# Kernel tuning notes

Measured on AMD Instinct MI355X. Metric: run time of the kernel, lower is better.

The kernel has to match this reference:

```python
import jax, jax.numpy as jnp
import numpy as np

B, T, V, S, I, G = 2, 4096, 1024, 256, 2048, 128


def setup_inputs() -> dict:
    key = jax.random.key(0)
    ks = jax.random.split(key, 10)
    n = lambda k, shape, std: jax.random.normal(k, shape, dtype=jnp.float32) * std
    return {
        "x": jax.random.normal(ks[0], (B, T, V), dtype=jnp.float32),
        # shared CausalMemory projections (torch Linear weight layout [out,in])
        "Wq": n(ks[1], (S, V), 0.02),
        "Wk": n(ks[2], (S, V), 0.02),
        "Wv": n(ks[3], (S, V), 0.02),
        "Wo": n(ks[4], (V, S), 0.02),
        # Delta
        "delta_logits": jnp.full((V,), 4.0, dtype=jnp.float32),
        "delta_scale": jnp.float32(0.1),
        # Theta / Gamma decay params
        "theta_decay": jnp.float32(4.0),
        "theta_scale": jnp.float32(0.1),
        "gamma_decay": jnp.float32(1.0),
        "gamma_scale": jnp.float32(0.1),
        # Alpha gate
        "alpha_down": n(ks[5], (G, V), 0.02),
        "alpha_up": n(ks[6], (V, G), 0.01),
        "alpha_up_b": jnp.full((V,), 2.0, dtype=jnp.float32),
        # Beta MLP
        "beta_down": n(ks[7], (I, V), 0.02),
        "beta_up": n(ks[8], (V, I), 0.02),
        "beta_bias": jnp.zeros((I,), dtype=jnp.float32),
        "beta_scale": jnp.float32(0.1),
    }


def _rmsnorm(x):
    eps = jnp.finfo(x.dtype).eps
    return x * jax.lax.rsqrt(jnp.mean(x * x, axis=-1, keepdims=True) + eps)


def _delta(x, decay_logits, scale):
    # causal EMA via weighted cumsum, matching torch reference exactly
    t = x.shape[1]
    decay = jax.nn.sigmoid(decay_logits)
    log_decay = jnp.log(jnp.clip(decay, 1e-06))
    steps = jnp.arange(t, dtype=x.dtype)[::-1]            # [T]
    w = jnp.exp(steps[:, None] * log_decay[None, :])      # [T,V]
    cum = jnp.cumsum(x * w[None], axis=1)
    cum = jnp.concatenate([jnp.zeros_like(cum[:, :1]), cum[:, :-1]], axis=1)
    return cum / jnp.clip(w[None], 1e-08) * scale


def _memory(x, Wq, Wk, Wv, Wo, decay_logit, scale):
    t = x.shape[1]
    q = x @ Wq.T
    k = x @ Wk.T
    v = x @ Wv.T
    scores = jnp.einsum("btd,bsd->bts", q, k)             # [B,T,T]
    decay = jax.nn.sigmoid(decay_logit)
    pos = jnp.arange(t)
    diff = pos[None, :] - pos[:, None]                    # j - i
    w = decay ** jnp.clip(diff.astype(x.dtype) - 1.0, 0.0, None) * (diff > 0)
    retrieved = jnp.einsum("bts,bsd->btd", scores * w[None], v)
    return (retrieved @ Wo.T) * scale


def _alpha(x, down, up, up_b):
    gate = jax.nn.sigmoid((x @ down.T) @ up.T + up_b)
    return x * gate


def _beta(x, down, up, bias, scale):
    h = jax.nn.gelu(x @ down.T + bias, approximate=False)
    return (h @ up.T) * scale


def reference(x, Wq, Wk, Wv, Wo, delta_logits, delta_scale, theta_decay,
              theta_scale, gamma_decay, gamma_scale, alpha_down, alpha_up,
              alpha_up_b, beta_down, beta_up, beta_bias, beta_scale):
    x = x + _delta(_rmsnorm(x), delta_logits, delta_scale)
    x = x + _memory(_rmsnorm(x), Wq, Wk, Wv, Wo, theta_decay, theta_scale)
    x = _alpha(x, alpha_down, alpha_up, alpha_up_b)
    x = x + _beta(_rmsnorm(x), beta_down, beta_up, beta_bias, beta_scale)
    x = x + _memory(_rmsnorm(x), Wq, Wk, Wv, Wo, gamma_decay, gamma_scale)
    return x
```

## Files before the change

### kernel.cpp

```cpp
#include <hip/hip_runtime.h>

typedef __attribute__((ext_vector_type(8))) short s16x8;
typedef __attribute__((ext_vector_type(4))) float f32x4;
typedef unsigned short u16;

#define DEV __device__ __forceinline__

DEV u16 f2b(float f) {
  unsigned u = __builtin_bit_cast(unsigned, f);
  unsigned r = (u + 0x7FFFu + ((u >> 16) & 1u)) >> 16;
  return (u16)r;
}
DEV float b2f(u16 h) { return __builtin_bit_cast(float, (unsigned)h << 16); }
DEV f32x4 mfma16(s16x8 a, s16x8 b, f32x4 c) {
  return __builtin_amdgcn_mfma_f32_16x16x32_bf16(a, b, c, 0, 0, 0);
}
DEV float sigmoidf_(float x) { return 1.0f / (1.0f + expf(-x)); }

DEV void g2l16(const u16* g, u16* l) {
  __builtin_amdgcn_global_load_lds((const __attribute__((address_space(1))) void*)g,
                                   (__attribute__((address_space(3))) void*)l, 16, 0, 0);
}

#define BAR() __builtin_amdgcn_s_barrier()
#define WAITV8() asm volatile("s_waitcnt vmcnt(8)" ::: "memory")
#define WAITV4() asm volatile("s_waitcnt vmcnt(4)" ::: "memory")
#define WAITV0() asm volatile("s_waitcnt vmcnt(0)" ::: "memory")
#define WAITL0()                                         \
  do {                                                   \
    asm volatile("s_waitcnt lgkmcnt(0)" ::: "memory");   \
    __builtin_amdgcn_sched_barrier(0);                   \
  } while (0)

__global__ __launch_bounds__(256) void cast_all(
    const float* __restrict__ Wq, const float* __restrict__ Wk, const float* __restrict__ Wv,
    const float* __restrict__ Wo, const float* __restrict__ adw, const float* __restrict__ auw,
    const float* __restrict__ bdw, const float* __restrict__ buw,
    u16* __restrict__ Wqkvb, u16* __restrict__ Wob, u16* __restrict__ adb,
    u16* __restrict__ aub, u16* __restrict__ bdb, u16* __restrict__ bub) {
  const int b = blockIdx.x;
  const float* s;
  u16* d;
  int rb;
  if (b < 768) {
    s = (b < 256) ? Wq : (b < 512) ? Wk : Wv;
    rb = (b < 256) ? b : (b < 512) ? (b - 256) : (b - 512);
    d = Wqkvb + ((b < 256) ? 0 : (b < 512) ? 262144 : 524288);
  } else if (b < 1024) { s = Wo;  d = Wob; rb = b - 768; }
  else if (b < 1152)   { s = adw; d = adb; rb = b - 1024; }
  else if (b < 1280)   { s = auw; d = aub; rb = b - 1152; }
  else if (b < 3328)   { s = bdw; d = bdb; rb = b - 1280; }
  else                 { s = buw; d = bub; rb = b - 3328; }
  size_t i = ((size_t)rb * 256 + threadIdx.x) * 4;
  float4 v = *(const float4*)(s + i);
  ushort4 p; p.x = f2b(v.x); p.y = f2b(v.y); p.z = f2b(v.z); p.w = f2b(v.w);
  *(ushort4*)(d + i) = p;
}

__global__ __launch_bounds__(256) void rmsnorm_k(const float* __restrict__ x, u16* __restrict__ y) {
  const size_t row = blockIdx.x;
  const int tid = threadIdx.x;
  float4 v = ((const float4*)(x + row * 1024))[tid];
  float ss = v.x * v.x + v.y * v.y + v.z * v.z + v.w * v.w;
#pragma unroll
  for (int o = 32; o >= 1; o >>= 1) ss += __shfl_xor(ss, o);
  __shared__ float red[4];
  if ((tid & 63) == 0) red[tid >> 6] = ss;
  __syncthreads();
  float tot = red[0] + red[1] + red[2] + red[3];
  float rn = rsqrtf(tot * (1.0f / 1024.0f) + 1.1920929e-7f);
  ushort4 p;
  p.x = f2b(v.x * rn); p.y = f2b(v.y * rn); p.z = f2b(v.z * rn); p.w = f2b(v.w * rn);
  *(ushort4*)(y + row * 1024 + tid * 4) = p;
}

__global__ __launch_bounds__(256)
void delta_partial(const u16* __restrict__ y, const float* __restrict__ logits, float* __restrict__ Pp) {
  const int v = blockIdx.x * 256 + threadIdx.x;
  const int c = blockIdx.y, b = blockIdx.z;
  const float dec = sigmoidf_(logits[v]);
  const float ldc = logf(fmaxf(dec, 1e-6f));
  const float dc = expf(ldc);
  const u16* yp = y + ((size_t)b * 4096 + c * 128) * 1024 + v;
  float wv = expf((float)(4095 - (c * 128 + 127)) * ldc);
  float acc = 0.0f;
  for (int t = 127; t >= 0; --t) {
    acc += b2f(yp[(size_t)t * 1024]) * wv;
    wv *= dc;
  }
  Pp[((size_t)b * 32 + c) * 1024 + v] = acc;
}

__global__ __launch_bounds__(256) void delta_scan(float* __restrict__ Pp) {
  const int v = blockIdx.x * 256 + threadIdx.x;
  const int b = blockIdx.y;
  float run = 0.0f;
  for (int c = 0; c < 32; ++c) {
    size_t i = ((size_t)b * 32 + c) * 1024 + v;
    float t = Pp[i];
    Pp[i] = run;
    run += t;
  }
}

__global__ __launch_bounds__(256)
void delta_apply(const float* __restrict__ x0, const u16* __restrict__ y,
                 const float* __restrict__ logits, const float* __restrict__ scale_p,
                 const float* __restrict__ Pp, float* __restrict__ x1) {
  const int v = blockIdx.x * 256 + threadIdx.x;
  const int c = blockIdx.y, b = blockIdx.z;
  const float dec = sigmoidf_(logits[v]);
  const float ldc = logf(fmaxf(dec, 1e-6f));
  const float dc = expf(ldc);
  const float invd = expf(-ldc);
  const float sc = scale_p[0];
  float wv = expf((float)(4095 - c * 128) * ldc);
  float iw = expf(-(float)(4095 - c * 128) * ldc);
  float carry = Pp[((size_t)b * 32 + c) * 1024 + v];
  size_t base = ((size_t)b * 4096 + c * 128) * 1024 + v;
  for (int t = 0; t < 128; ++t) {
    size_t idx = base + (size_t)t * 1024;
    x1[idx] = x0[idx] + carry * fminf(iw, 1e8f) * sc;
    carry += b2f(y[idx]) * wv;
    wv *= invd;
    iw *= dc;
  }
}

template <int EPI>
__global__ __launch_bounds__(256, 4)
void pgemm_s(const u16* __restrict__ A, const u16* __restrict__ Bw,
             int M, int N, int K,
             u16* __restrict__ Cb,
             const float* __restrict__ Xin, float* __restrict__ Xout,
             u16* __restrict__ Xb16,
             const float* __restrict__ bias, const float* __restrict__ scale_p,
             u16* __restrict__ P1, u16* __restrict__ P2, u16* __restrict__ P3) {
  __shared__ u16 sm[17472];
  const int tid = threadIdx.x;
  const int wid = tid >> 6, lane = tid & 63;
  const int gx = gridDim.x;
  const int id = blockIdx.y * gx + blockIdx.x;
  const int q8 = (gx * gridDim.y) >> 3;
  const int nid = (id & 7) * q8 + (id >> 3);
  const int bx = nid % gx, by = nid / gx;
  const int n0 = bx * 128, m0 = by * 128;
  const int wm = (wid >> 1) * 64, wn = (wid & 1) * 64;
  const int lr = lane & 15, lkc = lane >> 4;
  const int sw = lr & 7;
  const int c0 = (lkc ^ sw) * 8, c1 = ((lkc + 4) ^ sw) * 8;
  const int NT = K >> 6;
  const int srow = lane >> 3;
  const int scol = ((lane & 7) ^ srow) * 8;
  const u16* Ag = A + (size_t)(m0 + wid * 8 + srow) * K + scol;
  const u16* Bg = Bw + (size_t)(n0 + wid * 8 + srow) * K + scol;
  u16* const As = sm;
  u16* const Bs = sm + 8192;

  f32x4 acc[4][4] = {};

  for (int t = 0; t < NT; ++t) {
    {
      const u16* ga = Ag + (size_t)t * 64;
      const u16* gb = Bg + (size_t)t * 64;
      u16* la = As + wid * 512;
      u16* lb = Bs + wid * 512;
#pragma unroll
      for (int c = 0; c < 4; ++c) {
        g2l16(ga + (size_t)c * 32 * K, la + c * 2048);
        g2l16(gb + (size_t)c * 32 * K, lb + c * 2048);
      }
    }
    __syncthreads();
    s16x8 af[4][2], bfr[2][2][2];
#pragma unroll
    for (int i = 0; i < 4; ++i) {
      int base = (wm + i * 16 + lr) * 64;
      af[i][0] = *(const s16x8*)&As[base + c0];
      af[i][1] = *(const s16x8*)&As[base + c1];
    }
#pragma unroll
    for (int h = 0; h < 2; ++h)
#pragma unroll
      for (int j = 0; j < 2; ++j) {
        int base = (wn + h * 32 + j * 16 + lr) * 64;
        bfr[h][j][0] = *(const s16x8*)&Bs[base + c0];
        bfr[h][j][1] = *(const s16x8*)&Bs[base + c1];
      }
#pragma unroll
    for (int i = 0; i < 4; ++i)
#pragma unroll
      for (int h = 0; h < 2; ++h)
#pragma unroll
        for (int j = 0; j < 2; ++j) {
          acc[i][h * 2 + j] = mfma16(af[i][0], bfr[h][j][0], acc[i][h * 2 + j]);
          acc[i][h * 2 + j] = mfma16(af[i][1], bfr[h][j][1], acc[i][h * 2 + j]);
        }
    __syncthreads();
  }

  float* tl = (float*)(void*)sm + wid * 1088;

  if constexpr (EPI == 5) {
    if (bx < 4) {
      u16* dst = (bx < 2) ? Cb : P1;
      const int nb = (bx & 1) * 128;
#pragma unroll
      for (int i = 0; i < 4; ++i) {
#pragma unroll
        for (int j = 0; j < 4; ++j)
#pragma unroll
          for (int r = 0; r < 4; ++r)
            tl[(lkc * 4 + r) * 68 + j * 16 + lr] = acc[i][j][r];
#pragma unroll
        for (int p = 0; p < 4; ++p) {
          const int row = p * 4 + lkc, nl = lr * 4;
          f32x4 v = *(const f32x4*)&tl[row * 68 + nl];
          const int m = m0 + wm + i * 16 + row;
          ushort4 o = {f2b(v[0]), f2b(v[1]), f2b(v[2]), f2b(v[3])};
          *(ushort4*)&dst[(size_t)m * 256 + nb + wn + nl] = o;
        }
      }
      if (bx >= 2) {
        const float ld5 = logf(sigmoidf_(scale_p[0]));
        u16* CT = sm;
        __syncthreads();
#pragma unroll
        for (int i = 0; i < 4; ++i)
#pragma unroll
          for (int j = 0; j < 4; ++j)
#pragma unroll
            for (int r = 0; r < 4; ++r) {
              int ml = wm + i * 16 + lkc * 4 + r;
              int nl = wn + j * 16 + lr;
              float g = expf(ld5 * (float)(ml & 63));
              CT[nl * 136 + ml] = f2b(acc[i][j][r] * g);
            }
        __syncthreads();
        int d = tid >> 1, off = (tid & 1) * 64;
        size_t base = ((size_t)(m0 >> 12) * 256 + (bx - 2) * 128 + d) * 4096 + (m0 & 4095) + off;
#pragma unroll
        for (int p = 0; p < 8; ++p)
          *(uint4*)&P3[base + p * 8] = *(const uint4*)&CT[d * 136 + off + p * 8];
      }
    } else {
      u16* CT = sm;
      __syncthreads();
#pragma unroll
      for (int i = 0; i < 4; ++i)
#pragma unroll
        for (int j = 0; j < 4; ++j)
#pragma unroll
          for (int r = 0; r < 4; ++r) {
            int ml = wm + i * 16 + lkc * 4 + r;
            int nl = wn + j * 16 + lr;
            CT[nl * 136 + ml] = f2b(acc[i][j][r]);
          }
      __syncthreads();
      int d = tid >> 1, off = (tid & 1) * 64;
      size_t base = ((size_t)(m0 >> 12) * 256 + (bx - 4) * 128 + d) * 4096 + (m0 & 4095) + off;
#pragma unroll
      for (int p = 0; p < 8; ++p)
        *(uint4*)&P2[base + p * 8] = *(const uint4*)&CT[d * 136 + off + p * 8];
    }
  } else {
    const float sc = (EPI == 2) ? scale_p[0] : 0.0f;
    float4 bpf = {0.0f, 0.0f, 0.0f, 0.0f};
    if constexpr (EPI == 3 || EPI == 4) bpf = *(const float4*)&bias[n0 + wn + lr * 4];
#pragma unroll
    for (int i = 0; i < 4; ++i) {
#pragma unroll
      for (int j = 0; j < 4; ++j)
#pragma unroll
        for (int r = 0; r < 4; ++r)
          tl[(lkc * 4 + r) * 68 + j * 16 + lr] = acc[i][j][r];
#pragma unroll
      for (int p = 0; p < 4; ++p) {
        const int row = p * 4 + lkc, nl = lr * 4;
        f32x4 v = *(const f32x4*)&tl[row * 68 + nl];
        const int m = m0 + wm + i * 16 + row;
        const int n = n0 + wn + nl;
        const size_t idx = (size_t)m * N + n;
        if constexpr (EPI == 0) {
          ushort4 o = {f2b(v[0]), f2b(v[1]), f2b(v[2]), f2b(v[3])};
          *(ushort4*)&Cb[idx] = o;
        } else if constexpr (EPI == 2) {
          float4 x = *(const float4*)&Xin[idx];
          float4 o = {x.x + v[0] * sc, x.y + v[1] * sc, x.z + v[2] * sc, x.w + v[3] * sc};
          *(float4*)&Xout[idx] = o;
          if (Xb16) {
            ushort4 ob = {f2b(o.x), f2b(o.y), f2b(o.z), f2b(o.w)};
            *(ushort4*)&Xb16[idx] = ob;
          }
        } else if constexpr (EPI == 3) {
          float g0 = v[0] + bpf.x, g1 = v[1] + bpf.y, g2 = v[2] + bpf.z, g3 = v[3] + bpf.w;
          ushort4 o;
          o.x = f2b(g0 * sigmoidf_(1.59576912f * fmaf(0.044715f * g0, g0 * g0, g0)));
          o.y = f2b(g1 * sigmoidf_(1.59576912f * fmaf(0.044715f * g1, g1 * g1, g1)));
          o.z = f2b(g2 * sigmoidf_(1.59576912f * fmaf(0.044715f * g2, g2 * g2, g2)));
          o.w = f2b(g3 * sigmoidf_(1.59576912f * fmaf(0.044715f * g3, g3 * g3, g3)));
          *(ushort4*)&Cb[idx] = o;
        } else {
          float4 x = *(const float4*)&Xin[idx];
          float4 o = {x.x * sigmoidf_(v[0] + bpf.x), x.y * sigmoidf_(v[1] + bpf.y),
                      x.z * sigmoidf_(v[2] + bpf.z), x.w * sigmoidf_(v[3] + bpf.w)};
          *(float4*)&Xout[idx] = o;
        }
      }
    }
  }
}

template <int EPI>
__global__ __launch_bounds__(256, 2)
void pgemm_d(const u16* __restrict__ A, const u16* __restrict__ Bw,
             int M, int N, int K,
             u16* __restrict__ Cb,
             const float* __restrict__ Xin, float* __restrict__ Xout,
             u16* __restrict__ Xb16,
             const float* __restrict__ bias, const float* __restrict__ scale_p) {
  __shared__ u16 sm[32768];
  const int tid = threadIdx.x;
  const int wid = tid >> 6, lane = tid & 63;
  const int gx = gridDim.x;
  const int id = blockIdx.y * gx + blockIdx.x;
  const int q8 = (gx * gridDim.y) >> 3;
  const int nid = (id & 7) * q8 + (id >> 3);
  const int bx = nid % gx, by = nid / gx;
  const int n0 = bx * 128, m0 = by * 128;
  const int wm = (wid >> 1) * 64, wn = (wid & 1) * 64;
  const int lr = lane & 15, lkc = lane >> 4;
  const int sw = lr & 7;
  const int c0 = (lkc ^ sw) * 8, c1 = ((lkc + 4) ^ sw) * 8;
  const int NT = K >> 6;
  const int srow = lane >> 3;
  const int scol = ((lane & 7) ^ srow) * 8;
  const u16* Ag = A + (size_t)(m0 + wid * 8 + srow) * K + scol;
  const u16* Bg = Bw + (size_t)(n0 + wid * 8 + srow) * K + scol;
  u16* const AL0 = sm;          u16* const BL0 = sm + 8192;
  u16* const AL1 = sm + 16384;  u16* const BL1 = sm + 24576;

  f32x4 acc[4][4] = {};

  auto STA = [&](int tau) {
    const u16* g = Ag + (size_t)tau * 64;
    u16* l = ((tau & 1) ? AL1 : AL0) + wid * 512;
#pragma unroll
    for (int c = 0; c < 4; ++c) g2l16(g + (size_t)c * 32 * K, l + c * 2048);
  };
  auto STB = [&](int tau) {
    const u16* g = Bg + (size_t)tau * 64;
    u16* l = ((tau & 1) ? BL1 : BL0) + wid * 512;
#pragma unroll
    for (int c = 0; c < 4; ++c) g2l16(g + (size_t)c * 32 * K, l + c * 2048);
  };
  auto RDA = [&](int tau, s16x8 (&d)[4][2]) {
    const u16* Ab = (tau & 1) ? AL1 : AL0;
#pragma unroll
    for (int i = 0; i < 4; ++i) {
      int base = (wm + i * 16 + lr) * 64;
      d[i][0] = *(const s16x8*)&Ab[base + c0];
      d[i][1] = *(const s16x8*)&Ab[base + c1];
    }
  };
  auto RDB = [&](int tau, int h, s16x8 (&d)[2][2]) {
    const u16* Bb = (tau & 1) ? BL1 : BL0;
#pragma unroll
    for (int j = 0; j < 2; ++j) {
      int base = (wn + h * 32 + j * 16 + lr) * 64;
      d[j][0] = *(const s16x8*)&Bb[base + c0];
      d[j][1] = *(const s16x8*)&Bb[base + c1];
    }
  };
  auto MM = [&](s16x8 (&Ar)[4][2], s16x8 (&Br)[2][2], int jo) {
    __builtin_amdgcn_s_setprio(1);
#pragma unroll
    for (int i = 0; i < 4; ++i)
#pragma unroll
      for (int j = 0; j < 2; ++j) {
        acc[i][jo + j] = mfma16(Ar[i][0], Br[j][0], acc[i][jo + j]);
        acc[i][jo + j] = mfma16(Ar[i][1], Br[j][1], acc[i][jo + j]);
      }
    __builtin_amdgcn_s_setprio(0);
  };

  s16x8 Ae[4][2], Ao[4][2], B0r[2][2], B1r[2][2];
  STA(0); STB(0);
  if (NT > 1) { STA(1); STB(1); }
  WAITV8(); BAR();
  RDA(0, Ae); RDB(0, 0, B0r);

  for (int t = 0; t < NT; t += 2) {
    RDB(t, 1, B1r);
    if (t + 2 < NT) STA(t + 2);
    BAR(); WAITL0();
    MM(Ae, B0r, 0);
    BAR();
    if (t + 2 < NT) { STB(t + 2); WAITV8(); } else { WAITV0(); }
    BAR();
    if (t + 1 < NT) { RDA(t + 1, Ao); RDB(t + 1, 0, B0r); }
    WAITL0();
    MM(Ae, B1r, 2);
    BAR();
    if (t + 1 >= NT) break;
    RDB(t + 1, 1, B1r);
    if (t + 3 < NT) STA(t + 3);
    BAR(); WAITL0();
    MM(Ao, B0r, 0);
    BAR();
    if (t + 3 < NT) { STB(t + 3); WAITV8(); } else { WAITV0(); }
    BAR();
    if (t + 2 < NT) { RDA(t + 2, Ae); RDB(t + 2, 0, B0r); }
    WAITL0();
    MM(Ao, B1r, 2);
    BAR();
  }

  float* tl = (float*)(void*)sm + wid * 1088;
  const float sc = (EPI == 2) ? scale_p[0] : 0.0f;
  float4 bpf = {0.0f, 0.0f, 0.0f, 0.0f};
  if constexpr (EPI == 3 || EPI == 4) bpf = *(const float4*)&bias[n0 + wn + lr * 4];
#pragma unroll
  for (int i = 0; i < 4; ++i) {
#pragma unroll
    for (int j = 0; j < 4; ++j)
#pragma unroll
      for (int r = 0; r < 4; ++r)
        tl[(lkc * 4 + r) * 68 + j * 16 + lr] = acc[i][j][r];
#pragma unroll
    for (int p = 0; p < 4; ++p) {
      const int row = p * 4 + lkc, nl = lr * 4;
      f32x4 v = *(const f32x4*)&tl[row * 68 + nl];
      const int m = m0 + wm + i * 16 + row;
      const int n = n0 + wn + nl;
      const size_t idx = (size_t)m * N + n;
      if constexpr (EPI == 0) {
        ushort4 o = {f2b(v[0]), f2b(v[1]), f2b(v[2]), f2b(v[3])};
        *(ushort4*)&Cb[idx] = o;
      } else if constexpr (EPI == 2) {
        float4 x = *(const float4*)&Xin[idx];
        float4 o = {x.x + v[0] * sc, x.y + v[1] * sc, x.z + v[2] * sc, x.w + v[3] * sc};
        *(float4*)&Xout[idx] = o;
        if (Xb16) {
          ushort4 ob = {f2b(o.x), f2b(o.y), f2b(o.z), f2b(o.w)};
          *(ushort4*)&Xb16[idx] = ob;
        }
      } else if constexpr (EPI == 3) {
        float g0 = v[0] + bpf.x, g1 = v[1] + bpf.y, g2 = v[2] + bpf.z, g3 = v[3] + bpf.w;
        ushort4 o;
        o.x = f2b(g0 * sigmoidf_(1.59576912f * fmaf(0.044715f * g0, g0 * g0, g0)));
        o.y = f2b(g1 * sigmoidf_(1.59576912f * fmaf(0.044715f * g1, g1 * g1, g1)));
        o.z = f2b(g2 * sigmoidf_(1.59576912f * fmaf(0.044715f * g2, g2 * g2, g2)));
        o.w = f2b(g3 * sigmoidf_(1.59576912f * fmaf(0.044715f * g3, g3 * g3, g3)));
        *(ushort4*)&Cb[idx] = o;
      } else {
        float4 x = *(const float4*)&Xin[idx];
        float4 o = {x.x * sigmoidf_(v[0] + bpf.x), x.y * sigmoidf_(v[1] + bpf.y),
                    x.z * sigmoidf_(v[2] + bpf.z), x.w * sigmoidf_(v[3] + bpf.w)};
        *(float4*)&Xout[idx] = o;
      }
    }
  }
}

__global__ __launch_bounds__(256, 2)
void chunk_G(const u16* __restrict__ vT, const u16* __restrict__ kTs, float* __restrict__ Gp) {
  __shared__ u16 sm2[16384];
  const int c = blockIdx.x, eh = blockIdx.y >> 1, dh = blockIdx.y & 1, b = blockIdx.z;
  const int tid = threadIdx.x, wid = tid >> 6, lane = tid & 63;
  u16* AL = sm2; u16* BL = sm2 + 8192;
  const u16* As = vT + (size_t)(b * 256 + eh * 128) * 4096 + c * 64;
  const u16* Bs = kTs + (size_t)(b * 256 + dh * 128) * 4096 + c * 64;
  const int r8 = lane >> 3, sc8 = ((lane & 7) ^ (lane >> 3)) * 8;
#pragma unroll
  for (int p = 0; p < 4; ++p) {
    int ch = p * 4 + wid;
    int row = ch * 8 + r8;
    g2l16(As + (size_t)row * 4096 + sc8, AL + ch * 512);
    g2l16(Bs + (size_t)row * 4096 + sc8, BL + ch * 512);
  }
  __syncthreads();
  const int wm = (wid >> 1) * 64, wn = (wid & 1) * 64;
  const int lr = lane & 15, lkc = lane >> 4, sw = lr & 7;
  const int c0 = (lkc ^ sw) * 8, c1 = ((lkc + 4) ^ sw) * 8;
  s16x8 af[4][2], bf[4][2];
#pragma unroll
  for (int i = 0; i < 4; ++i) {
    int ba = (wm + i * 16 + lr) * 64;
    af[i][0] = *(const s16x8*)&AL[ba + c0];
    af[i][1] = *(const s16x8*)&AL[ba + c1];
    int bb = (wn + i * 16 + lr) * 64;
    bf[i][0] = *(const s16x8*)&BL[bb + c0];
    bf[i][1] = *(const s16x8*)&BL[bb + c1];
  }
  f32x4 acc[4][4] = {};
#pragma unroll
  for (int i = 0; i < 4; ++i)
#pragma unroll
    for (int j = 0; j < 4; ++j) {
      acc[i][j] = mfma16(af[i][0], bf[j][0], acc[i][j]);
      acc[i][j] = mfma16(af[i][1], bf[j][1], acc[i][j]);
    }
  float* Gb = Gp + (size_t)(b * 64 + c) * 65536;
#pragma unroll
  for (int i = 0; i < 4; ++i)
#pragma unroll
    for (int j = 0; j < 4; ++j)
#pragma unroll
      for (int r = 0; r < 4; ++r) {
        int e = eh * 128 + wm + i * 16 + lkc * 4 + r;
        int d = dh * 128 + wn + j * 16 + lr;
        Gb[(size_t)e * 256 + d] = acc[i][j][r];
      }
}

__global__ __launch_bounds__(256)
void scan_M(const float* __restrict__ Gp, u16* __restrict__ Mb, const float* __restrict__ dlogit) {
  const int b = blockIdx.y;
  const size_t idx = (size_t)blockIdx.x * 256 + threadIdx.x;
  const float ld = logf(sigmoidf_(dlogit[0]));
  const float g64 = expf(64.0f * ld);
  const float* G = Gp + (size_t)b * 64 * 65536 + idx;
  u16* M = Mb + (size_t)b * 64 * 65536 + idx;
  float m = 0.0f;
  M[(size_t)63 * 65536] = 0;
  float g = G[(size_t)63 * 65536];
  for (int c = 62; c >= 0; --c) {
    float gn = 0.0f;
    if (c > 0) gn = G[(size_t)c * 65536];
    m = g + g64 * m;
    M[(size_t)c * 65536] = f2b(m);
    g = gn;
  }
}

__global__ __launch_bounds__(256, 2)
void chunk_R(const u16* __restrict__ q, const u16* __restrict__ k,
             const u16* __restrict__ vT, const u16* __restrict__ Mb,
             u16* __restrict__ R, const float* __restrict__ dlogit) {
  __shared__ u16 qL[16384];
  __shared__ u16 shA[16384];
  const int c = blockIdx.x, eh = blockIdx.y, b = blockIdx.z;
  const int tid = threadIdx.x, wid = tid >> 6, lane = tid & 63;
  const float ld = logf(sigmoidf_(dlogit[0]));
  const int r8 = lane >> 3, sc8 = ((lane & 7) ^ (lane >> 3)) * 8;
  const int lr = lane & 15, lkc = lane >> 4, g4 = lkc * 4;
  const int sw = lr & 7;
  const int c0 = (lkc ^ sw) * 8, c1 = ((lkc + 4) ^ sw) * 8;

  const u16* qsrc = q + ((size_t)b * 4096 + c * 64) * 256;
  const u16* ksrc = k + ((size_t)b * 4096 + c * 64) * 256;
  const u16* msrc = Mb + ((size_t)(b * 64 + c) * 256 + eh * 128) * 256;
  const u16* vsrc = vT + (size_t)(b * 256 + eh * 128) * 4096 + c * 64;

#pragma unroll
  for (int kt = 0; kt < 4; ++kt)
#pragma unroll
    for (int p = 0; p < 2; ++p) {
      int ch = p * 4 + wid;
      int row = ch * 8 + r8;
      g2l16(qsrc + (size_t)row * 256 + kt * 64 + sc8, qL + kt * 4096 + ch * 512);
    }
#pragma unroll
  for (int p = 0; p < 4; ++p) {
    int ch = p * 4 + wid;
    int row = ch * 8 + r8;
    g2l16(msrc + (size_t)row * 256 + sc8, shA + ch * 512);
  }
  f32x4 accx[4][2] = {};
  for (int dt = 0; dt < 4; ++dt) {
    if (dt < 3) {
      u16* dst = shA + ((dt + 1) & 1) * 8192;
#pragma unroll
      for (int p = 0; p < 4; ++p) {
        int ch = p * 4 + wid;
        int row = ch * 8 + r8;
        g2l16(msrc + (size_t)row * 256 + (dt + 1) * 64 + sc8, dst + ch * 512);
      }
      WAITV4();
    } else {
      WAITV0();
    }
    BAR();
    const u16* mt = shA + (dt & 1) * 8192;
    const u16* qt = qL + dt * 4096;
    s16x8 aq[4][2], bm[2][2];
#pragma unroll
    for (int i = 0; i < 4; ++i) {
      int ba = (i * 16 + lr) * 64;
      aq[i][0] = *(const s16x8*)&qt[ba + c0];
      aq[i][1] = *(const s16x8*)&qt[ba + c1];
    }
#pragma unroll
    for (int j = 0; j < 2; ++j) {
      int ba = (wid * 32 + j * 16 + lr) * 64;
      bm[j][0] = *(const s16x8*)&mt[ba + c0];
      bm[j][1] = *(const s16x8*)&mt[ba + c1];
    }
#pragma unroll
    for (int i = 0; i < 4; ++i)
#pragma unroll
      for (int j = 0; j < 2; ++j) {
        accx[i][j] = mfma16(aq[i][0], bm[j][0], accx[i][j]);
        accx[i][j] = mfma16(aq[i][1], bm[j][1], accx[i][j]);
      }
    BAR();
  }
#pragma unroll
  for (int kt = 0; kt < 4; ++kt)
#pragma unroll
    for (int p = 0; p < 2; ++p) {
      int ch = p * 4 + wid;
      int row = ch * 8 + r8;
      g2l16(ksrc + (size_t)row * 256 + kt * 64 + sc8, shA + kt * 4096 + ch * 512);
    }
  __syncthreads();
  f32x4 accs[4] = {};
#pragma unroll
  for (int kt = 0; kt < 4; ++kt) {
    const u16* qt = qL + kt * 4096;
    const u16* klt = shA + kt * 4096;
    s16x8 aq[4][2], bk[2];
#pragma unroll
    for (int i = 0; i < 4; ++i) {
      int ba = (i * 16 + lr) * 64;
      aq[i][0] = *(const s16x8*)&qt[ba + c0];
      aq[i][1] = *(const s16x8*)&qt[ba + c1];
    }
    {
      int ba = (wid * 16 + lr) * 64;
      bk[0] = *(const s16x8*)&klt[ba + c0];
      bk[1] = *(const s16x8*)&klt[ba + c1];
    }
#pragma unroll
    for (int i = 0; i < 4; ++i) {
      accs[i] = mfma16(aq[i][0], bk[0], accs[i]);
      accs[i] = mfma16(aq[i][1], bk[1], accs[i]);
    }
  }
  __syncthreads();
  u16* PL = shA;
  u16* vTL = shA + 4608;
#pragma unroll
  for (int p = 0; p < 4; ++p) {
    int ch = p * 4 + wid;
    int row = ch * 8 + r8;
    g2l16(vsrc + (size_t)row * 4096 + sc8, vTL + ch * 512);
  }
#pragma unroll
  for (int i = 0; i < 4; ++i)
#pragma unroll
    for (int r = 0; r < 4; ++r) {
      int gi = i * 16 + g4 + r;
      int gj = wid * 16 + lr;
      float pw = (gj > gi) ? expf(ld * (float)(gj - gi - 1)) : 0.0f;
      PL[gi * 72 + gj] = f2b(accs[i][r] * pw);
    }
  __syncthreads();
  f32x4 acci[4][2] = {};
  {
    s16x8 pa[4][2], bv[2][2];
#pragma unroll
    for (int i = 0; i < 4; ++i) {
      pa[i][0] = *(const s16x8*)&PL[(i * 16 + lr) * 72 + lkc * 8];
      pa[i][1] = *(const s16x8*)&PL[(i * 16 + lr) * 72 + 32 + lkc * 8];
    }
#pragma unroll
    for (int j = 0; j < 2; ++j) {
      int ba = (wid * 32 + j * 16 + lr) * 64;
      bv[j][0] = *(const s16x8*)&vTL[ba + c0];
      bv[j][1] = *(const s16x8*)&vTL[ba + c1];
    }
#pragma unroll
    for (int i = 0; i < 4; ++i)
#pragma unroll
      for (int j = 0; j < 2; ++j) {
        acci[i][j] = mfma16(pa[i][0], bv[j][0], acci[i][j]);
        acci[i][j] = mfma16(pa[i][1], bv[j][1], acci[i][j]);
      }
  }
  u16* Ro = R + ((size_t)b * 4096 + c * 64) * 256 + eh * 128;
#pragma unroll
  for (int i = 0; i < 4; ++i)
#pragma unroll
    for (int r = 0; r < 4; ++r) {
      int gi = i * 16 + g4 + r;
      float xf = expf(ld * (float)(63 - gi));
#pragma unroll
      for (int j = 0; j < 2; ++j) {
        int ge = wid * 32 + j * 16 + lr;
        Ro[(size_t)gi * 256 + ge] = f2b(acci[i][j][r] + xf * accx[i][j][r]);
      }
    }
}

extern "C" void kernel_launch(void* const* d_in, const int* in_sizes, int n_in,
                              void* d_out, int out_size, void* d_ws, size_t ws_size,
                              hipStream_t stream) {
  const float* x0 = (const float*)d_in[0];
  const float* Wq = (const float*)d_in[1];
  const float* Wk = (const float*)d_in[2];
  const float* Wv = (const float*)d_in[3];
  const float* Wo = (const float*)d_in[4];
  const float* dlog = (const float*)d_in[5];
  const float* dscale = (const float*)d_in[6];
  const float* th_dec = (const float*)d_in[7];
  const float* th_sc = (const float*)d_in[8];
  const float* ga_dec = (const float*)d_in[9];
  const float* ga_sc = (const float*)d_in[10];
  const float* adw = (const float*)d_in[11];
  const float* auw = (const float*)d_in[12];
  const float* a_upb = (const float*)d_in[13];
  const float* bdw = (const float*)d_in[14];
  const float* buw = (const float*)d_in[15];
  const float* bbias = (const float*)d_in[16];
  const float* bscale = (const float*)d_in[17];

  char* w = (char*)d_ws;
  float* xA = (float*)w;
  u16* y = (u16*)(w + 33554432);
  u16* xb = (u16*)(w + 50331648);
  u16* qb = (u16*)(w + 67108864);
  u16* kb = (u16*)(w + 71303168);
  u16* vT = (u16*)(w + 75497472);
  u16* Rb = (u16*)(w + 79691776);
  u16* gb = (u16*)(w + 83886080);
  u16* hb = (u16*)(w + 85983232);
  float* Gp = (float*)hb;
  u16* Mbuf = y;
  u16* kTs = xb;
  float* Pp = (float*)(w + 119537664);
  u16* Wqkvb = (u16*)(w + 119799808);
  u16* Wob = (u16*)(w + 121372672);
  u16* adb = (u16*)(w + 121896960);
  u16* aub = (u16*)(w + 122159104);
  u16* bdb = (u16*)(w + 122421248);
  u16* bub = (u16*)(w + 126615552);
  float* xB = (float*)d_out;

  cast_all<<<5376, 256, 0, stream>>>(Wq, Wk, Wv, Wo, adw, auw, bdw, buw,
                                     Wqkvb, Wob, adb, aub, bdb, bub);

  rmsnorm_k<<<8192, 256, 0, stream>>>(x0, y);
  delta_partial<<<dim3(4, 32, 2), 256, 0, stream>>>(y, dlog, Pp);
  delta_scan<<<dim3(4, 2), 256, 0, stream>>>(Pp);
  delta_apply<<<dim3(4, 32, 2), 256, 0, stream>>>(x0, y, dlog, dscale, Pp, xA);

  rmsnorm_k<<<8192, 256, 0, stream>>>(xA, y);
  pgemm_s<5><<<dim3(6, 64), 256, 0, stream>>>(y, Wqkvb, 8192, 768, 1024, qb, nullptr, nullptr, nullptr, nullptr, th_dec, kb, vT, kTs);
  chunk_G<<<dim3(64, 4, 2), 256, 0, stream>>>(vT, kTs, Gp);
  scan_M<<<dim3(256, 2), 256, 0, stream>>>(Gp, Mbuf, th_dec);
  chunk_R<<<dim3(64, 2, 2), 256, 0, stream>>>(qb, kb, vT, Mbuf, Rb, th_dec);
  pgemm_d<2><<<dim3(8, 64), 256, 0, stream>>>(Rb, Wob, 8192, 1024, 256, nullptr, xA, xB, xb, nullptr, th_sc);

  pgemm_s<0><<<dim3(1, 64), 256, 0, stream>>>(xb, adb, 8192, 128, 1024, gb, nullptr, nullptr, nullptr, nullptr, nullptr, nullptr, nullptr, nullptr);
  pgemm_d<4><<<dim3(8, 64), 256, 0, stream>>>(gb, aub, 8192, 1024, 128, nullptr, xB, xA, nullptr, a_upb, nullptr);

  rmsnorm_k<<<8192, 256, 0, stream>>>(xA, y);
  pgemm_s<3><<<dim3(16, 64), 256, 0, stream>>>(y, bdb, 8192, 2048, 1024, hb, nullptr, nullptr, nullptr, bbias, nullptr, nullptr, nullptr, nullptr);
  pgemm_s<2><<<dim3(8, 64), 256, 0, stream>>>(hb, bub, 8192, 1024, 2048, nullptr, xA, xB, nullptr, nullptr, bscale, nullptr, nullptr, nullptr);

  rmsnorm_k<<<8192, 256, 0, stream>>>(xB, y);
  pgemm_s<5><<<dim3(6, 64), 256, 0, stream>>>(y, Wqkvb, 8192, 768, 1024, qb, nullptr, nullptr, nullptr, nullptr, ga_dec, kb, vT, kTs);
  chunk_G<<<dim3(64, 4, 2), 256, 0, stream>>>(vT, kTs, Gp);
  scan_M<<<dim3(256, 2), 256, 0, stream>>>(Gp, Mbuf, ga_dec);
  chunk_R<<<dim3(64, 2, 2), 256, 0, stream>>>(qb, kb, vT, Mbuf, Rb, ga_dec);
  pgemm_d<2><<<dim3(8, 64), 256, 0, stream>>>(Rb, Wob, 8192, 1024, 256, nullptr, xB, xB, nullptr, nullptr, ga_sc);
}
```

Baseline: 342.7 us.

## Store chunk G partials in bf16 and route QKV/alpha-down GEMMs to double-buffered kernel

The chunk_G partial products are now written as bf16 instead of fp32, halving the traffic of that intermediate read by scan_M. The fused QKV projection epilogue (EPI 5) and the alpha-down GEMM move from the single-buffered pgemm_s kernel to the double-buffered pgemm_d kernel, which uses global-to-LDS loads with a ping-pong schedule. This trades occupancy (2 blocks per CU instead of 4, larger LDS footprint) for overlap of loads with MFMA, and adds bf16 rounding error to the G partials before the scan.

```diff
diff --git a/kernel.cpp b/kernel.cpp
--- a/kernel.cpp
+++ b/kernel.cpp
@@ -134,8 +134,7 @@
              u16* __restrict__ Cb,
              const float* __restrict__ Xin, float* __restrict__ Xout,
              u16* __restrict__ Xb16,
-             const float* __restrict__ bias, const float* __restrict__ scale_p,
-             u16* __restrict__ P1, u16* __restrict__ P2, u16* __restrict__ P3) {
+             const float* __restrict__ bias, const float* __restrict__ scale_p) {
   __shared__ u16 sm[17472];
   const int tid = threadIdx.x;
   const int wid = tid >> 6, lane = tid & 63;
@@ -197,6 +196,159 @@
           acc[i][h * 2 + j] = mfma16(af[i][1], bfr[h][j][1], acc[i][h * 2 + j]);
         }
     __syncthreads();
+  }
+
+  float* tl = (float*)(void*)sm + wid * 1088;
+  const float sc = (EPI == 2) ? scale_p[0] : 0.0f;
+  float4 bpf = {0.0f, 0.0f, 0.0f, 0.0f};
+  if constexpr (EPI == 3 || EPI == 4) bpf = *(const float4*)&bias[n0 + wn + lr * 4];
+#pragma unroll
+  for (int i = 0; i < 4; ++i) {
+#pragma unroll
+    for (int j = 0; j < 4; ++j)
+#pragma unroll
+      for (int r = 0; r < 4; ++r)
+        tl[(lkc * 4 + r) * 68 + j * 16 + lr] = acc[i][j][r];
+#pragma unroll
+    for (int p = 0; p < 4; ++p) {
+      const int row = p * 4 + lkc, nl = lr * 4;
+      f32x4 v = *(const f32x4*)&tl[row * 68 + nl];
+      const int m = m0 + wm + i * 16 + row;
+      const int n = n0 + wn + nl;
+      const size_t idx = (size_t)m * N + n;
+      if constexpr (EPI == 0) {
+        ushort4 o = {f2b(v[0]), f2b(v[1]), f2b(v[2]), f2b(v[3])};
+        *(ushort4*)&Cb[idx] = o;
+      } else if constexpr (EPI == 2) {
+        float4 x = *(const float4*)&Xin[idx];
+        float4 o = {x.x + v[0] * sc, x.y + v[1] * sc, x.z + v[2] * sc, x.w + v[3] * sc};
+        *(float4*)&Xout[idx] = o;
+        if (Xb16) {
+          ushort4 ob = {f2b(o.x), f2b(o.y), f2b(o.z), f2b(o.w)};
+          *(ushort4*)&Xb16[idx] = ob;
+        }
+      } else if constexpr (EPI == 3) {
+        float g0 = v[0] + bpf.x, g1 = v[1] + bpf.y, g2 = v[2] + bpf.z, g3 = v[3] + bpf.w;
+        ushort4 o;
+        o.x = f2b(g0 * sigmoidf_(1.59576912f * fmaf(0.044715f * g0, g0 * g0, g0)));
+        o.y = f2b(g1 * sigmoidf_(1.59576912f * fmaf(0.044715f * g1, g1 * g1, g1)));
+        o.z = f2b(g2 * sigmoidf_(1.59576912f * fmaf(0.044715f * g2, g2 * g2, g2)));
+        o.w = f2b(g3 * sigmoidf_(1.59576912f * fmaf(0.044715f * g3, g3 * g3, g3)));
+        *(ushort4*)&Cb[idx] = o;
+      } else {
+        float4 x = *(const float4*)&Xin[idx];
+        float4 o = {x.x * sigmoidf_(v[0] + bpf.x), x.y * sigmoidf_(v[1] + bpf.y),
+                    x.z * sigmoidf_(v[2] + bpf.z), x.w * sigmoidf_(v[3] + bpf.w)};
+        *(float4*)&Xout[idx] = o;
+      }
+    }
+  }
+}
+
+template <int EPI>
+__global__ __launch_bounds__(256, 2)
+void pgemm_d(const u16* __restrict__ A, const u16* __restrict__ Bw,
+             int M, int N, int K,
+             u16* __restrict__ Cb,
+             const float* __restrict__ Xin, float* __restrict__ Xout,
+             u16* __restrict__ Xb16,
+             const float* __restrict__ bias, const float* __restrict__ scale_p,
+             u16* __restrict__ P1, u16* __restrict__ P2, u16* __restrict__ P3) {
+  __shared__ u16 sm[32768];
+  const int tid = threadIdx.x;
+  const int wid = tid >> 6, lane = tid & 63;
+  const int gx = gridDim.x;
+  const int id = blockIdx.y * gx + blockIdx.x;
+  const int q8 = (gx * gridDim.y) >> 3;
+  const int nid = (id & 7) * q8 + (id >> 3);
+  const int bx = nid % gx, by = nid / gx;
+  const int n0 = bx * 128, m0 = by * 128;
+  const int wm = (wid >> 1) * 64, wn = (wid & 1) * 64;
+  const int lr = lane & 15, lkc = lane >> 4;
+  const int sw = lr & 7;
+  const int c0 = (lkc ^ sw) * 8, c1 = ((lkc + 4) ^ sw) * 8;
+  const int NT = K >> 6;
+  const int srow = lane >> 3;
+  const int scol = ((lane & 7) ^ srow) * 8;
+  const u16* Ag = A + (size_t)(m0 + wid * 8 + srow) * K + scol;
+  const u16* Bg = Bw + (size_t)(n0 + wid * 8 + srow) * K + scol;
+  u16* const AL0 = sm;          u16* const BL0 = sm + 8192;
+  u16* const AL1 = sm + 16384;  u16* const BL1 = sm + 24576;
+
+  f32x4 acc[4][4] = {};
+
+  auto STA = [&](int tau) {
+    const u16* g = Ag + (size_t)tau * 64;
+    u16* l = ((tau & 1) ? AL1 : AL0) + wid * 512;
+#pragma unroll
+    for (int c = 0; c < 4; ++c) g2l16(g + (size_t)c * 32 * K, l + c * 2048);
+  };
+  auto STB = [&](int tau) {
+    const u16* g = Bg + (size_t)tau * 64;
+    u16* l = ((tau & 1) ? BL1 : BL0) + wid * 512;
+#pragma unroll
+    for (int c = 0; c < 4; ++c) g2l16(g + (size_t)c * 32 * K, l + c * 2048);
+  };
+  auto RDA = [&](int tau, s16x8 (&d)[4][2]) {
+    const u16* Ab = (tau & 1) ? AL1 : AL0;
+#pragma unroll
+    for (int i = 0; i < 4; ++i) {
+      int base = (wm + i * 16 + lr) * 64;
+      d[i][0] = *(const s16x8*)&Ab[base + c0];
+      d[i][1] = *(const s16x8*)&Ab[base + c1];
+    }
+  };
+  auto RDB = [&](int tau, int h, s16x8 (&d)[2][2]) {
+    const u16* Bb = (tau & 1) ? BL1 : BL0;
+#pragma unroll
+    for (int j = 0; j < 2; ++j) {
+      int base = (wn + h * 32 + j * 16 + lr) * 64;
+      d[j][0] = *(const s16x8*)&Bb[base + c0];
+      d[j][1] = *(const s16x8*)&Bb[base + c1];
+    }
+  };
+  auto MM = [&](s16x8 (&Ar)[4][2], s16x8 (&Br)[2][2], int jo) {
+    __builtin_amdgcn_s_setprio(1);
+#pragma unroll
+    for (int i = 0; i < 4; ++i)
+#pragma unroll
+      for (int j = 0; j < 2; ++j) {
+        acc[i][jo + j] = mfma16(Ar[i][0], Br[j][0], acc[i][jo + j]);
+        acc[i][jo + j] = mfma16(Ar[i][1], Br[j][1], acc[i][jo + j]);
+      }
+    __builtin_amdgcn_s_setprio(0);
+  };
+
+  s16x8 Ae[4][2], Ao[4][2], B0r[2][2], B1r[2][2];
+  STA(0); STB(0);
+  if (NT > 1) { STA(1); STB(1); }
+  WAITV8(); BAR();
+  RDA(0, Ae); RDB(0, 0, B0r);
+
+  for (int t = 0; t < NT; t += 2) {
+    RDB(t, 1, B1r);
+    if (t + 2 < NT) STA(t + 2);
+    BAR(); WAITL0();
+    MM(Ae, B0r, 0);
+    BAR();
+    if (t + 2 < NT) { STB(t + 2); WAITV8(); } else { WAITV0(); }
+    BAR();
+    if (t + 1 < NT) { RDA(t + 1, Ao); RDB(t + 1, 0, B0r); }
+    WAITL0();
+    MM(Ae, B1r, 2);
+    BAR();
+    if (t + 1 >= NT) break;
+    RDB(t + 1, 1, B1r);
+    if (t + 3 < NT) STA(t + 3);
+    BAR(); WAITL0();
+    MM(Ao, B0r, 0);
+    BAR();
+    if (t + 3 < NT) { STB(t + 3); WAITV8(); } else { WAITV0(); }
+    BAR();
+    if (t + 2 < NT) { RDA(t + 2, Ae); RDB(t + 2, 0, B0r); }
+    WAITL0();
+    MM(Ao, B1r, 2);
+    BAR();
   }
 
   float* tl = (float*)(void*)sm + wid * 1088;
@@ -311,160 +463,8 @@
   }
 }
 
-template <int EPI>
 __global__ __launch_bounds__(256, 2)
-void pgemm_d(const u16* __restrict__ A, const u16* __restrict__ Bw,
-             int M, int N, int K,
-             u16* __restrict__ Cb,
-             const float* __restrict__ Xin, float* __restrict__ Xout,
-             u16* __restrict__ Xb16,
-             const float* __restrict__ bias, const float* __restrict__ scale_p) {
-  __shared__ u16 sm[32768];
-  const int tid = threadIdx.x;
-  const int wid = tid >> 6, lane = tid & 63;
-  const int gx = gridDim.x;
-  const int id = blockIdx.y * gx + blockIdx.x;
-  const int q8 = (gx * gridDim.y) >> 3;
-  const int nid = (id & 7) * q8 + (id >> 3);
-  const int bx = nid % gx, by = nid / gx;
-  const int n0 = bx * 128, m0 = by * 128;
-  const int wm = (wid >> 1) * 64, wn = (wid & 1) * 64;
-  const int lr = lane & 15, lkc = lane >> 4;
-  const int sw = lr & 7;
-  const int c0 = (lkc ^ sw) * 8, c1 = ((lkc + 4) ^ sw) * 8;
-  const int NT = K >> 6;
-  const int srow = lane >> 3;
-  const int scol = ((lane & 7) ^ srow) * 8;
-  const u16* Ag = A + (size_t)(m0 + wid * 8 + srow) * K + scol;
-  const u16* Bg = Bw + (size_t)(n0 + wid * 8 + srow) * K + scol;
-  u16* const AL0 = sm;          u16* const BL0 = sm + 8192;
-  u16* const AL1 = sm + 16384;  u16* const BL1 = sm + 24576;
-
-  f32x4 acc[4][4] = {};
-
-  auto STA = [&](int tau) {
-    const u16* g = Ag + (size_t)tau * 64;
-    u16* l = ((tau & 1) ? AL1 : AL0) + wid * 512;
-#pragma unroll
-    for (int c = 0; c < 4; ++c) g2l16(g + (size_t)c * 32 * K, l + c * 2048);
-  };
-  auto STB = [&](int tau) {
-    const u16* g = Bg + (size_t)tau * 64;
-    u16* l = ((tau & 1) ? BL1 : BL0) + wid * 512;
-#pragma unroll
-    for (int c = 0; c < 4; ++c) g2l16(g + (size_t)c * 32 * K, l + c * 2048);
-  };
-  auto RDA = [&](int tau, s16x8 (&d)[4][2]) {
-    const u16* Ab = (tau & 1) ? AL1 : AL0;
-#pragma unroll
-    for (int i = 0; i < 4; ++i) {
-      int base = (wm + i * 16 + lr) * 64;
-      d[i][0] = *(const s16x8*)&Ab[base + c0];
-      d[i][1] = *(const s16x8*)&Ab[base + c1];
-    }
-  };
-  auto RDB = [&](int tau, int h, s16x8 (&d)[2][2]) {
-    const u16* Bb = (tau & 1) ? BL1 : BL0;
-#pragma unroll
-    for (int j = 0; j < 2; ++j) {
-      int base = (wn + h * 32 + j * 16 + lr) * 64;
-      d[j][0] = *(const s16x8*)&Bb[base + c0];
-      d[j][1] = *(const s16x8*)&Bb[base + c1];
-    }
-  };
-  auto MM = [&](s16x8 (&Ar)[4][2], s16x8 (&Br)[2][2], int jo) {
-    __builtin_amdgcn_s_setprio(1);
-#pragma unroll
-    for (int i = 0; i < 4; ++i)
-#pragma unroll
-      for (int j = 0; j < 2; ++j) {
-        acc[i][jo + j] = mfma16(Ar[i][0], Br[j][0], acc[i][jo + j]);
-        acc[i][jo + j] = mfma16(Ar[i][1], Br[j][1], acc[i][jo + j]);
-      }
-    __builtin_amdgcn_s_setprio(0);
-  };
-
-  s16x8 Ae[4][2], Ao[4][2], B0r[2][2], B1r[2][2];
-  STA(0); STB(0);
-  if (NT > 1) { STA(1); STB(1); }
-  WAITV8(); BAR();
-  RDA(0, Ae); RDB(0, 0, B0r);
-
-  for (int t = 0; t < NT; t += 2) {
-    RDB(t, 1, B1r);
-    if (t + 2 < NT) STA(t + 2);
-    BAR(); WAITL0();
-    MM(Ae, B0r, 0);
-    BAR();
-    if (t + 2 < NT) { STB(t + 2); WAITV8(); } else { WAITV0(); }
-    BAR();
-    if (t + 1 < NT) { RDA(t + 1, Ao); RDB(t + 1, 0, B0r); }
-    WAITL0();
-    MM(Ae, B1r, 2);
-    BAR();
-    if (t + 1 >= NT) break;
-    RDB(t + 1, 1, B1r);
-    if (t + 3 < NT) STA(t + 3);
-    BAR(); WAITL0();
-    MM(Ao, B0r, 0);
-    BAR();
-    if (t + 3 < NT) { STB(t + 3); WAITV8(); } else { WAITV0(); }
-    BAR();
-    if (t + 2 < NT) { RDA(t + 2, Ae); RDB(t + 2, 0, B0r); }
-    WAITL0();
-    MM(Ao, B1r, 2);
-    BAR();
-  }
-
-  float* tl = (float*)(void*)sm + wid * 1088;
-  const float sc = (EPI == 2) ? scale_p[0] : 0.0f;
-  float4 bpf = {0.0f, 0.0f, 0.0f, 0.0f};
-  if constexpr (EPI == 3 || EPI == 4) bpf = *(const float4*)&bias[n0 + wn + lr * 4];
-#pragma unroll
-  for (int i = 0; i < 4; ++i) {
-#pragma unroll
-    for (int j = 0; j < 4; ++j)
-#pragma unroll
-      for (int r = 0; r < 4; ++r)
-        tl[(lkc * 4 + r) * 68 + j * 16 + lr] = acc[i][j][r];
-#pragma unroll
-    for (int p = 0; p < 4; ++p) {
-      const int row = p * 4 + lkc, nl = lr * 4;
-      f32x4 v = *(const f32x4*)&tl[row * 68 + nl];
-      const int m = m0 + wm + i * 16 + row;
-      const int n = n0 + wn + nl;
-      const size_t idx = (size_t)m * N + n;
-      if constexpr (EPI == 0) {
-        ushort4 o = {f2b(v[0]), f2b(v[1]), f2b(v[2]), f2b(v[3])};
-        *(ushort4*)&Cb[idx] = o;
-      } else if constexpr (EPI == 2) {
-        float4 x = *(const float4*)&Xin[idx];
-        float4 o = {x.x + v[0] * sc, x.y + v[1] * sc, x.z + v[2] * sc, x.w + v[3] * sc};
-        *(float4*)&Xout[idx] = o;
-        if (Xb16) {
-          ushort4 ob = {f2b(o.x), f2b(o.y), f2b(o.z), f2b(o.w)};
-          *(ushort4*)&Xb16[idx] = ob;
-        }
-      } else if constexpr (EPI == 3) {
-        float g0 = v[0] + bpf.x, g1 = v[1] + bpf.y, g2 = v[2] + bpf.z, g3 = v[3] + bpf.w;
-        ushort4 o;
-        o.x = f2b(g0 * sigmoidf_(1.59576912f * fmaf(0.044715f * g0, g0 * g0, g0)));
-        o.y = f2b(g1 * sigmoidf_(1.59576912f * fmaf(0.044715f * g1, g1 * g1, g1)));
-        o.z = f2b(g2 * sigmoidf_(1.59576912f * fmaf(0.044715f * g2, g2 * g2, g2)));
-        o.w = f2b(g3 * sigmoidf_(1.59576912f * fmaf(0.044715f * g3, g3 * g3, g3)));
-        *(ushort4*)&Cb[idx] = o;
-      } else {
-        float4 x = *(const float4*)&Xin[idx];
-        float4 o = {x.x * sigmoidf_(v[0] + bpf.x), x.y * sigmoidf_(v[1] + bpf.y),
-                    x.z * sigmoidf_(v[2] + bpf.z), x.w * sigmoidf_(v[3] + bpf.w)};
-        *(float4*)&Xout[idx] = o;
-      }
-    }
-  }
-}
-
-__global__ __launch_bounds__(256, 2)
-void chunk_G(const u16* __restrict__ vT, const u16* __restrict__ kTs, float* __restrict__ Gp) {
+void chunk_G(const u16* __restrict__ vT, const u16* __restrict__ kTs, u16* __restrict__ Gp) {
   __shared__ u16 sm2[16384];
   const int c = blockIdx.x, eh = blockIdx.y >> 1, dh = blockIdx.y & 1, b = blockIdx.z;
   const int tid = threadIdx.x, wid = tid >> 6, lane = tid & 63;
@@ -501,7 +501,7 @@
       acc[i][j] = mfma16(af[i][0], bf[j][0], acc[i][j]);
       acc[i][j] = mfma16(af[i][1], bf[j][1], acc[i][j]);
     }
-  float* Gb = Gp + (size_t)(b * 64 + c) * 65536;
+  u16* Gb = Gp + (size_t)(b * 64 + c) * 65536;
 #pragma unroll
   for (int i = 0; i < 4; ++i)
 #pragma unroll
@@ -510,24 +510,24 @@
       for (int r = 0; r < 4; ++r) {
         int e = eh * 128 + wm + i * 16 + lkc * 4 + r;
         int d = dh * 128 + wn + j * 16 + lr;
-        Gb[(size_t)e * 256 + d] = acc[i][j][r];
+        Gb[(size_t)e * 256 + d] = f2b(acc[i][j][r]);
       }
 }
 
 __global__ __launch_bounds__(256)
-void scan_M(const float* __restrict__ Gp, u16* __restrict__ Mb, const float* __restrict__ dlogit) {
+void scan_M(const u16* __restrict__ Gp, u16* __restrict__ Mb, const float* __restrict__ dlogit) {
   const int b = blockIdx.y;
   const size_t idx = (size_t)blockIdx.x * 256 + threadIdx.x;
   const float ld = logf(sigmoidf_(dlogit[0]));
   const float g64 = expf(64.0f * ld);
-  const float* G = Gp + (size_t)b * 64 * 65536 + idx;
+  const u16* G = Gp + (size_t)b * 64 * 65536 + idx;
   u16* M = Mb + (size_t)b * 64 * 65536 + idx;
   float m = 0.0f;
   M[(size_t)63 * 65536] = 0;
-  float g = G[(size_t)63 * 65536];
+  float g = b2f(G[(size_t)63 * 65536]);
   for (int c = 62; c >= 0; --c) {
     float gn = 0.0f;
-    if (c > 0) gn = G[(size_t)c * 65536];
+    if (c > 0) gn = b2f(G[(size_t)c * 65536]);
     m = g + g64 * m;
     M[(size_t)c * 65536] = f2b(m);
     g = gn;
@@ -726,7 +726,7 @@
   u16* Rb = (u16*)(w + 79691776);
   u16* gb = (u16*)(w + 83886080);
   u16* hb = (u16*)(w + 85983232);
-  float* Gp = (float*)hb;
+  u16* Gp = hb;
   u16* Mbuf = y;
   u16* kTs = xb;
   float* Pp = (float*)(w + 119537664);
@@ -747,23 +747,23 @@
   delta_apply<<<dim3(4, 32, 2), 256, 0, stream>>>(x0, y, dlog, dscale, Pp, xA);
 
   rmsnorm_k<<<8192, 256, 0, stream>>>(xA, y);
-  pgemm_s<5><<<dim3(6, 64), 256, 0, stream>>>(y, Wqkvb, 8192, 768, 1024, qb, nullptr, nullptr, nullptr, nullptr, th_dec, kb, vT, kTs);
+  pgemm_d<5><<<dim3(6, 64), 256, 0, stream>>>(y, Wqkvb, 8192, 768, 1024, qb, nullptr, nullptr, nullptr, nullptr, th_dec, kb, vT, kTs);
   chunk_G<<<dim3(64, 4, 2), 256, 0, stream>>>(vT, kTs, Gp);
   scan_M<<<dim3(256, 2), 256, 0, stream>>>(Gp, Mbuf, th_dec);
   chunk_R<<<dim3(64, 2, 2), 256, 0, stream>>>(qb, kb, vT, Mbuf, Rb, th_dec);
-  pgemm_d<2><<<dim3(8, 64), 256, 0, stream>>>(Rb, Wob, 8192, 1024, 256, nullptr, xA, xB, xb, nullptr, th_sc);
-
-  pgemm_s<0><<<dim3(1, 64), 256, 0, stream>>>(xb, adb, 8192, 128, 1024, gb, nullptr, nullptr, nullptr, nullptr, nullptr, nullptr, nullptr, nullptr);
-  pgemm_d<4><<<dim3(8, 64), 256, 0, stream>>>(gb, aub, 8192, 1024, 128, nullptr, xB, xA, nullptr, a_upb, nullptr);
+  pgemm_d<2><<<dim3(8, 64), 256, 0, stream>>>(Rb, Wob, 8192, 1024, 256, nullptr, xA, xB, xb, nullptr, th_sc, nullptr, nullptr, nullptr);
+
+  pgemm_d<0><<<dim3(1, 64), 256, 0, stream>>>(xb, adb, 8192, 128, 1024, gb, nullptr, nullptr, nullptr, nullptr, nullptr, nullptr, nullptr, nullptr);
+  pgemm_d<4><<<dim3(8, 64), 256, 0, stream>>>(gb, aub, 8192, 1024, 128, nullptr, xB, xA, nullptr, a_upb, nullptr, nullptr, nullptr, nullptr);
 
   rmsnorm_k<<<8192, 256, 0, stream>>>(xA, y);
-  pgemm_s<3><<<dim3(16, 64), 256, 0, stream>>>(y, bdb, 8192, 2048, 1024, hb, nullptr, nullptr, nullptr, bbias, nullptr, nullptr, nullptr, nullptr);
-  pgemm_s<2><<<dim3(8, 64), 256, 0, stream>>>(hb, bub, 8192, 1024, 2048, nullptr, xA, xB, nullptr, nullptr, bscale, nullptr, nullptr, nullptr);
+  pgemm_s<3><<<dim3(16, 64), 256, 0, stream>>>(y, bdb, 8192, 2048, 1024, hb, nullptr, nullptr, nullptr, bbias, nullptr);
+  pgemm_s<2><<<dim3(8, 64), 256, 0, stream>>>(hb, bub, 8192, 1024, 2048, nullptr, xA, xB, nullptr, nullptr, bscale);
 
   rmsnorm_k<<<8192, 256, 0, stream>>>(xB, y);
-  pgemm_s<5><<<dim3(6, 64), 256, 0, stream>>>(y, Wqkvb, 8192, 768, 1024, qb, nullptr, nullptr, nullptr, nullptr, ga_dec, kb, vT, kTs);
+  pgemm_d<5><<<dim3(6, 64), 256, 0, stream>>>(y, Wqkvb, 8192, 768, 1024, qb, nullptr, nullptr, nullptr, nullptr, ga_dec, kb, vT, kTs);
   chunk_G<<<dim3(64, 4, 2), 256, 0, stream>>>(vT, kTs, Gp);
   scan_M<<<dim3(256, 2), 256, 0, stream>>>(Gp, Mbuf, ga_dec);
   chunk_R<<<dim3(64, 2, 2), 256, 0, stream>>>(qb, kb, vT, Mbuf, Rb, ga_dec);
-  pgemm_d<2><<<dim3(8, 64), 256, 0, stream>>>(Rb, Wob, 8192, 1024, 256, nullptr, xB, xB, nullptr, nullptr, ga_sc);
-}
+  pgemm_d<2><<<dim3(8, 64), 256, 0, stream>>>(Rb, Wob, 8192, 1024, 256, nullptr, xB, xB, nullptr, nullptr, ga_sc, nullptr, nullptr, nullptr);
+}
```

After: 327.4 us. 4.5% less time.
